# Optimization experiments

Measured on AMD Instinct MI355X. Metric: run time of the kernel, lower is better.

## Reference

```python
import jax, jax.numpy as jnp
import numpy as np

V, E, H, D, A = 10000, 256, 256, 256, 256  # vocab, emb, enc_hid, dec_hid, attn_dim
B, S = 128, 64


def setup_inputs() -> dict:
    key = jax.random.key(0)
    ks = jax.random.split(key, 20)
    rn = lambda k, shp, sc: jax.random.normal(k, shp, jnp.float32) * sc
    tokens = jax.random.randint(ks[0], (B, S), 0, V, dtype=jnp.int32)
    inp = jnp.stack([tokens, jnp.ones_like(tokens)], axis=-1)  # [B,S,2], ch1 = mask
    s = 0.05
    return {
        "input": inp,
        "emb_table": rn(ks[1], (V, E), s),
        "enc_Wih_f": rn(ks[2], (3 * H, E), s), "enc_Whh_f": rn(ks[3], (3 * H, H), s),
        "enc_bih_f": rn(ks[4], (3 * H,), s), "enc_bhh_f": rn(ks[5], (3 * H,), s),
        "enc_Wih_b": rn(ks[6], (3 * H, E), s), "enc_Whh_b": rn(ks[7], (3 * H, H), s),
        "enc_bih_b": rn(ks[8], (3 * H,), s), "enc_bhh_b": rn(ks[9], (3 * H,), s),
        "enc_fc_W": rn(ks[10], (D, 2 * H), s), "enc_fc_b": rn(ks[11], (D,), s),
        "attn_W": rn(ks[12], (A, 2 * H + D), s), "attn_b": rn(ks[13], (A,), s),
        "dec_Wih": rn(ks[14], (3 * D, 2 * H + E), s), "dec_Whh": rn(ks[15], (3 * D, D), s),
        "dec_bih": rn(ks[16], (3 * D,), s), "dec_bhh": rn(ks[17], (3 * D,), s),
        "out_W": rn(ks[18], (V, 2 * H + D + E), s), "out_b": rn(ks[19], (V,), s),
    }


def _gru_cell(xp, h, Whh, bhh):
    # xp = x @ Wih.T + bih already computed; PyTorch gate order r,z,n
    rx, zx, nx = jnp.split(xp, 3, axis=-1)
    rh, zh, nh = jnp.split(h @ Whh.T + bhh, 3, axis=-1)
    r = jax.nn.sigmoid(rx + rh)
    z = jax.nn.sigmoid(zx + zh)
    n = jnp.tanh(nx + r * nh)
    return (1.0 - z) * n + z * h


def _gru_dir(x, Wih, Whh, bih, bhh, reverse):
    # x: [B,S,E] -> outputs [B,S,Hd], final hidden [B,Hd]
    xp = jnp.einsum('bse,ge->bsg', x, Wih) + bih  # [B,S,3Hd]
    Hd = Whh.shape[1]

    def step(h, xpt):
        h = _gru_cell(xpt, h, Whh, bhh)
        return h, h

    h0 = jnp.zeros((x.shape[0], Hd), x.dtype)
    hT, ys = jax.lax.scan(step, h0, jnp.swapaxes(xp, 0, 1), reverse=reverse)
    return jnp.swapaxes(ys, 0, 1), hT


def reference(input, emb_table, enc_Wih_f, enc_Whh_f, enc_bih_f, enc_bhh_f,
              enc_Wih_b, enc_Whh_b, enc_bih_b, enc_bhh_b, enc_fc_W, enc_fc_b,
              attn_W, attn_b, dec_Wih, dec_Whh, dec_bih, dec_bhh, out_W, out_b):
    b, s = input.shape[0], input.shape[1]
    v = emb_table.shape[0]
    tok = input[:, :, 0]
    mask = input[:, :, 1].astype(jnp.float32)
    emb = emb_table[tok] * mask[:, :, None]  # [B,S,E]

    # bidirectional encoder
    f_out, f_h = _gru_dir(emb, enc_Wih_f, enc_Whh_f, enc_bih_f, enc_bhh_f, False)
    b_out, b_h = _gru_dir(emb, enc_Wih_b, enc_Whh_b, enc_bih_b, enc_bhh_b, True)
    enc_out = jnp.concatenate([f_out, b_out], axis=-1)  # [B,S,2H]
    hidden = jnp.tanh(jnp.concatenate([f_h, b_h], axis=-1) @ enc_fc_W.T + enc_fc_b)  # [B,D]

    d = hidden.shape[1]

    def dec_step(carry, _):
        tok_t, h = carry
        e = emb_table[tok_t]  # [B,E]
        rep = jnp.concatenate(
            [jnp.broadcast_to(h[:, None, :], (b, s, d)), enc_out], axis=-1)
        energy = jnp.tanh(jnp.einsum('bsf,af->bsa', rep, attn_W) + attn_b)
        a = jax.nn.softmax(jnp.sum(energy, axis=-1), axis=1)  # [B,S]
        w = jnp.einsum('bs,bsh->bh', a, enc_out)  # [B,2H]
        rnn_in = jnp.concatenate([e, w], axis=-1)
        xp = rnn_in @ dec_Wih.T + dec_bih
        h_new = _gru_cell(xp, h, dec_Whh, dec_bhh)
        logits = jnp.concatenate([h_new, w, e], axis=-1) @ out_W.T + out_b  # [B,V]
        tok_new = jnp.argmax(logits, axis=-1).astype(tok_t.dtype)
        return (tok_new, h_new), logits

    tok0 = jnp.zeros((b,), jnp.int32)
    (_, _), outs = jax.lax.scan(dec_step, (tok0, hidden), None, length=s - 1)
    first = jnp.zeros((b, v), jnp.float32).at[:, 0].set(1.0)  # outputs[:,0] one-hot
    outputs = jnp.concatenate([first[:, None, :], jnp.swapaxes(outs, 0, 1)], axis=1)
    return jax.nn.log_softmax(outputs.reshape(-1, v), axis=-1)
```

## Files before the change

kernel.cpp:

```cpp
#include <hip/hip_runtime.h>
#include <math.h>


__device__ __forceinline__ float dot4(const float4 a, const float4 b) {
    return fmaf(a.x, b.x, fmaf(a.y, b.y, fmaf(a.z, b.z, a.w * b.w)));
}

__global__ void embed_kernel(const int* __restrict__ inp, const float* __restrict__ table,
                             float* __restrict__ emb) {
    int bs = blockIdx.x;
    int tok = inp[bs * 2];
    float msk = (float)inp[bs * 2 + 1];
    emb[bs * 256 + threadIdx.x] = table[tok * 256 + threadIdx.x] * msk;
}

__global__ __launch_bounds__(256) void enc_step_kernel(
    const float* __restrict__ emb,
    const float* __restrict__ Wih_f, const float* __restrict__ Whh_f,
    const float* __restrict__ bih_f, const float* __restrict__ bhh_f,
    const float* __restrict__ Wih_b, const float* __restrict__ Whh_b,
    const float* __restrict__ bih_b, const float* __restrict__ bhh_b,
    const float* __restrict__ hin_f, float* __restrict__ hout_f,
    const float* __restrict__ hin_b, float* __restrict__ hout_b,
    float* __restrict__ enc_out, int step)
{
    const int dir = blockIdx.y;
    const float* Wih = dir ? Wih_b : Wih_f;
    const float* Whh = dir ? Whh_b : Whh_f;
    const float* bih = dir ? bih_b : bih_f;
    const float* bhh = dir ? bhh_b : bhh_f;
    const float* hin = dir ? hin_b : hin_f;
    float* hout = dir ? hout_b : hout_f;
    const int t = dir ? (63 - step) : step;

    const int tid = threadIdx.x;
    const int dl = tid & 31;
    const int bsub = tid >> 5;
    const int d0 = (blockIdx.x & 7) * 32;
    const int b0 = (blockIdx.x >> 3) * 8;
    const int d = d0 + dl;
    const int b = b0 + bsub;

    __shared__ __align__(16) float xs[8][256];
    __shared__ __align__(16) float hs[8][256];
    for (int i = tid; i < 2048; i += 256) {
        int bl = i >> 8, e = i & 255;
        int bb = b0 + bl;
        xs[bl][e] = emb[(bb * 64 + t) * 256 + e];
        hs[bl][e] = hin[bb * 256 + e];
    }
    __syncthreads();

    const float4* x4 = (const float4*)xs[bsub];
    const float4* h4 = (const float4*)hs[bsub];
    const float4* wr_i = (const float4*)(Wih + (size_t)d * 256);
    const float4* wz_i = (const float4*)(Wih + (size_t)(256 + d) * 256);
    const float4* wn_i = (const float4*)(Wih + (size_t)(512 + d) * 256);
    const float4* wr_h = (const float4*)(Whh + (size_t)d * 256);
    const float4* wz_h = (const float4*)(Whh + (size_t)(256 + d) * 256);
    const float4* wn_h = (const float4*)(Whh + (size_t)(512 + d) * 256);

    float rs = 0.f, zs = 0.f, nx = 0.f, nh = 0.f;
    for (int k = 0; k < 64; ++k) {
        float4 xv = x4[k];
        float4 hv = h4[k];
        rs += dot4(xv, wr_i[k]) + dot4(hv, wr_h[k]);
        zs += dot4(xv, wz_i[k]) + dot4(hv, wz_h[k]);
        nx += dot4(xv, wn_i[k]);
        nh += dot4(hv, wn_h[k]);
    }
    rs += bih[d] + bhh[d];
    zs += bih[256 + d] + bhh[256 + d];
    nx += bih[512 + d];
    nh += bhh[512 + d];

    float r = 1.0f / (1.0f + expf(-rs));
    float z = 1.0f / (1.0f + expf(-zs));
    float n = tanhf(nx + r * nh);
    float hprev = hs[bsub][d];
    float hn = (1.0f - z) * n + z * hprev;

    hout[b * 256 + d] = hn;
    enc_out[(b * 64 + t) * 512 + dir * 256 + d] = hn;
}

__global__ __launch_bounds__(256) void enc_fc_kernel(
    const float* __restrict__ hf, const float* __restrict__ hb,
    const float* __restrict__ W, const float* __restrict__ bias,
    float* __restrict__ hdec0)
{
    int b = blockIdx.x, tid = threadIdx.x;
    __shared__ __align__(16) float xs[512];
    xs[tid] = hf[b * 256 + tid];
    xs[256 + tid] = hb[b * 256 + tid];
    __syncthreads();
    const float4* w4 = (const float4*)(W + (size_t)tid * 512);
    const float4* x4 = (const float4*)xs;
    float s = 0.f;
    for (int k = 0; k < 128; ++k) s += dot4(x4[k], w4[k]);
    hdec0[b * 256 + tid] = tanhf(s + bias[tid]);
}

#define GP 68
__global__ __launch_bounds__(256) void gemm2_kernel(
    const float* __restrict__ Amat, int lda,
    const float* __restrict__ Wmat, int ldw,
    const float* __restrict__ bias,
    float* __restrict__ C, long ldc,
    int N, int K)
{
    const int tid = threadIdx.x;
    const int tn = tid & 15;
    const int tm = tid >> 4;
    const long m0 = (long)blockIdx.y * 64;
    const int n0 = blockIdx.x * 64;
    __shared__ __align__(16) float As[64][GP];
    __shared__ __align__(16) float Ws[64][GP];

    const float* Abase = Amat + (m0 + tm) * lda + tn * 4;
    float4 ar[4], wr[4];
    float acc[4][4] = {};

    {
#pragma unroll
        for (int q = 0; q < 4; ++q)
            ar[q] = *(const float4*)(Abase + (long)16 * q * lda);
#pragma unroll
        for (int q = 0; q < 4; ++q) {
            int n = n0 + tm + 16 * q;
            wr[q] = (n < N) ? *(const float4*)(Wmat + (long)n * ldw + tn * 4)
                            : make_float4(0.f, 0.f, 0.f, 0.f);
        }
    }

    int k0 = 0;
    while (true) {
#pragma unroll
        for (int q = 0; q < 4; ++q) {
            *(float4*)&As[tm + 16 * q][tn * 4] = ar[q];
            *(float4*)&Ws[tm + 16 * q][tn * 4] = wr[q];
        }
        __syncthreads();

        const int kn = k0 + 64;
        if (kn < K) {
#pragma unroll
            for (int q = 0; q < 4; ++q)
                ar[q] = *(const float4*)(Abase + (long)16 * q * lda + kn);
#pragma unroll
            for (int q = 0; q < 4; ++q) {
                int n = n0 + tm + 16 * q;
                wr[q] = (n < N) ? *(const float4*)(Wmat + (long)n * ldw + tn * 4 + kn)
                                : make_float4(0.f, 0.f, 0.f, 0.f);
            }
        }

#pragma unroll
        for (int kk = 0; kk < 64; kk += 4) {
            float4 av[4], wv[4];
#pragma unroll
            for (int i = 0; i < 4; ++i) av[i] = *(const float4*)&As[tm + 16 * i][kk];
#pragma unroll
            for (int j = 0; j < 4; ++j) wv[j] = *(const float4*)&Ws[tn + 16 * j][kk];
#pragma unroll
            for (int i = 0; i < 4; ++i)
#pragma unroll
                for (int j = 0; j < 4; ++j)
                    acc[i][j] += dot4(av[i], wv[j]);
        }

        if (kn >= K) break;
        __syncthreads();
        k0 = kn;
    }

#pragma unroll
    for (int i = 0; i < 4; ++i) {
        long m = m0 + tm + 16 * i;
#pragma unroll
        for (int j = 0; j < 4; ++j) {
            int n = n0 + tn + 16 * j;
            if (n < N) C[m * ldc + n] = acc[i][j] + bias[n];
        }
    }
}

__global__ __launch_bounds__(256) void gemm80_kernel(
    const float* __restrict__ Amat, const float* __restrict__ Wmat,
    const float* __restrict__ bias, float* __restrict__ C)
{
    const int tid = threadIdx.x;
    const int tn = tid & 15;
    const int tm = tid >> 4;
    const long m0 = (long)blockIdx.y * 64;
    const int n0 = blockIdx.x * 80;
    __shared__ __align__(16) float As[64][GP];
    __shared__ __align__(16) float Ws[80][GP];

    const float* Abase = Amat + (m0 + tm) * 1024 + tn * 4;
    const float* Wbase = Wmat + (long)(n0 + tm) * 1024 + tn * 4;
    float4 ar[4], wr[5];
    float acc[4][5] = {};

    {
#pragma unroll
        for (int q = 0; q < 4; ++q)
            ar[q] = *(const float4*)(Abase + (long)16 * q * 1024);
#pragma unroll
        for (int q = 0; q < 5; ++q)
            wr[q] = *(const float4*)(Wbase + (long)16 * q * 1024);
    }

    int k0 = 0;
    while (true) {
#pragma unroll
        for (int q = 0; q < 4; ++q)
            *(float4*)&As[tm + 16 * q][tn * 4] = ar[q];
#pragma unroll
        for (int q = 0; q < 5; ++q)
            *(float4*)&Ws[tm + 16 * q][tn * 4] = wr[q];
        __syncthreads();

        const int kn = k0 + 64;
        if (kn < 1024) {
#pragma unroll
            for (int q = 0; q < 4; ++q)
                ar[q] = *(const float4*)(Abase + (long)16 * q * 1024 + kn);
#pragma unroll
            for (int q = 0; q < 5; ++q)
                wr[q] = *(const float4*)(Wbase + (long)16 * q * 1024 + kn);
        }

#pragma unroll
        for (int kk = 0; kk < 64; kk += 4) {
            float4 av[4], wv[5];
#pragma unroll
            for (int i = 0; i < 4; ++i) av[i] = *(const float4*)&As[tm + 16 * i][kk];
#pragma unroll
            for (int j = 0; j < 5; ++j) wv[j] = *(const float4*)&Ws[tn + 16 * j][kk];
#pragma unroll
            for (int i = 0; i < 4; ++i)
#pragma unroll
                for (int j = 0; j < 5; ++j)
                    acc[i][j] += dot4(av[i], wv[j]);
        }

        if (kn >= 1024) break;
        __syncthreads();
        k0 = kn;
    }

#pragma unroll
    for (int i = 0; i < 4; ++i) {
        long m = m0 + tm + 16 * i;
#pragma unroll
        for (int j = 0; j < 5; ++j) {
            int n = n0 + tn + 16 * j;
            C[m * 640000 + n] = acc[i][j] + bias[n];
        }
    }
}

__device__ __forceinline__ void attn_phase(
    int b, const float* __restrict__ hprev, const float* __restrict__ attn_W,
    const float* __restrict__ enc_att, const float* __restrict__ enc_out,
    float* __restrict__ feat,
    float* __restrict__ hsh, float* __restrict__ hE,
    float* __restrict__ part, float* __restrict__ aw)
{
    const int tid = threadIdx.x;
    hsh[tid] = hprev[b * 256 + tid];
    __syncthreads();
    {
        const float4* w4 = (const float4*)(attn_W + (size_t)tid * 768);
        const float4* h4 = (const float4*)hsh;
        float s = 0.f;
        for (int k = 0; k < 64; ++k) s += dot4(h4[k], w4[k]);
        hE[tid] = s;
    }
    __syncthreads();
    {
        const int si = tid & 63, g = tid >> 6;
        const float* ea = enc_att + ((size_t)b * 64 + si) * 256 + g * 64;
        const float* he = hE + g * 64;
        float p = 0.f;
        for (int a = 0; a < 64; ++a) p += tanhf(he[a] + ea[a]);
        part[tid] = p;
    }
    __syncthreads();
    if (tid < 64) {
        float sc = part[tid] + part[64 + tid] + part[128 + tid] + part[192 + tid];
        float m = sc;
        for (int off = 32; off; off >>= 1) m = fmaxf(m, __shfl_xor(m, off));
        float ex = expf(sc - m);
        float sum = ex;
        for (int off = 32; off; off >>= 1) sum += __shfl_xor(sum, off);
        aw[tid] = ex / sum;
    }
    __syncthreads();
    {
        float w0 = 0.f, w1 = 0.f;
        for (int s2 = 0; s2 < 64; ++s2) {
            float as = aw[s2];
            const float* eo = enc_out + ((size_t)b * 64 + s2) * 512;
            w0 = fmaf(as, eo[tid], w0);
            w1 = fmaf(as, eo[256 + tid], w1);
        }
        feat[b * 1024 + 256 + tid] = w0;
        feat[b * 1024 + 512 + tid] = w1;
    }
}

__global__ __launch_bounds__(256) void attn_kernel(
    const float* __restrict__ hprev, const float* __restrict__ attn_W,
    const float* __restrict__ enc_att, const float* __restrict__ enc_out,
    float* __restrict__ feat)
{
    __shared__ __align__(16) float hsh[256];
    __shared__ __align__(16) float hE[256];
    __shared__ __align__(16) float part[256];
    __shared__ __align__(16) float aw[64];
    attn_phase(blockIdx.x, hprev, attn_W, enc_att, enc_out, feat, hsh, hE, part, aw);
}

__device__ __forceinline__ void argmax_phase(
    int b, const float* __restrict__ logits, const float* __restrict__ table,
    int* __restrict__ tok, float* __restrict__ feat,
    float* __restrict__ bv, int* __restrict__ bix)
{
    const int tid = threadIdx.x;
    const float4* row4 = (const float4*)(logits + (long)b * 640000);
    float best = -3.402823466e38f;
    int bi = 0;
    for (int v4 = tid; v4 < 2500; v4 += 256) {
        float4 x = row4[v4];
        int base = v4 << 2;
        if (x.x > best) { best = x.x; bi = base; }
        if (x.y > best) { best = x.y; bi = base + 1; }
        if (x.z > best) { best = x.z; bi = base + 2; }
        if (x.w > best) { best = x.w; bi = base + 3; }
    }
    bv[tid] = best; bix[tid] = bi;
    __syncthreads();
    for (int s2 = 128; s2; s2 >>= 1) {
        if (tid < s2) {
            float o = bv[tid + s2]; int oi = bix[tid + s2];
            if (o > bv[tid] || (o == bv[tid] && oi < bix[tid])) { bv[tid] = o; bix[tid] = oi; }
        }
        __syncthreads();
    }
    int t0 = bix[0];
    if (tid == 0) tok[b] = t0;
    feat[b * 1024 + 768 + tid] = table[(size_t)t0 * 256 + tid];
}

__global__ __launch_bounds__(256) void post_kernel(
    const float* __restrict__ logits, const float* __restrict__ table,
    int* __restrict__ tok, float* __restrict__ feat,
    const float* __restrict__ hcur, const float* __restrict__ attn_W,
    const float* __restrict__ enc_att, const float* __restrict__ enc_out)
{
    __shared__ __align__(16) float s0[256];
    __shared__ __align__(16) float s1[256];
    __shared__ __align__(16) float s2[256];
    __shared__ __align__(16) float s3[64];
    __shared__ __align__(16) int   si[256];
    const int bid = blockIdx.x;
    if (bid < 128)
        argmax_phase(bid, logits, table, tok, feat, s0, si);
    else
        attn_phase(bid - 128, hcur, attn_W, enc_att, enc_out, feat, s0, s1, s2, s3);
}

__global__ __launch_bounds__(256) void dec_gru_kernel(
    const float* __restrict__ feat, const float* __restrict__ hin,
    const float* __restrict__ Wih, const float* __restrict__ Whh,
    const float* __restrict__ bih, const float* __restrict__ bhh,
    float* __restrict__ hout, float* __restrict__ feat_h)
{
    const int tid = threadIdx.x;
    const int dl = tid & 31, bsub = tid >> 5;
    const int d0 = (blockIdx.x & 7) * 32, b0 = (blockIdx.x >> 3) * 8;
    const int d = d0 + dl, b = b0 + bsub;

    __shared__ __align__(16) float rin[8][768];
    __shared__ __align__(16) float hsh[8][256];
    for (int i = tid; i < 2048; i += 256) {
        int bl = i >> 8, k = i & 255;
        rin[bl][k] = feat[(b0 + bl) * 1024 + 768 + k];
    }
    for (int i = tid; i < 4096; i += 256) {
        int bl = i >> 9, k = i & 511;
        rin[bl][256 + k] = feat[(b0 + bl) * 1024 + 256 + k];
    }
    for (int i = tid; i < 2048; i += 256) {
        int bl = i >> 8, k = i & 255;
        hsh[bl][k] = hin[(b0 + bl) * 256 + k];
    }
    __syncthreads();

    const float4* xv4 = (const float4*)rin[bsub];
    const float4* hv4 = (const float4*)hsh[bsub];
    const float4* Wr = (const float4*)(Wih + (size_t)d * 768);
    const float4* Wz = (const float4*)(Wih + (size_t)(256 + d) * 768);
    const float4* Wn = (const float4*)(Wih + (size_t)(512 + d) * 768);
    const float4* Ur = (const float4*)(Whh + (size_t)d * 256);
    const float4* Uz = (const float4*)(Whh + (size_t)(256 + d) * 256);
    const float4* Un = (const float4*)(Whh + (size_t)(512 + d) * 256);

    float rs = 0.f, zs = 0.f, nx = 0.f, nh = 0.f;
    for (int k = 0; k < 192; ++k) {
        float4 xv = xv4[k];
        rs += dot4(xv, Wr[k]);
        zs += dot4(xv, Wz[k]);
        nx += dot4(xv, Wn[k]);
    }
    for (int k = 0; k < 64; ++k) {
        float4 hv = hv4[k];
        rs += dot4(hv, Ur[k]);
        zs += dot4(hv, Uz[k]);
        nh += dot4(hv, Un[k]);
    }
    rs += bih[d] + bhh[d];
    zs += bih[256 + d] + bhh[256 + d];
    nx += bih[512 + d];
    nh += bhh[512 + d];

    float r = 1.0f / (1.0f + expf(-rs));
    float z = 1.0f / (1.0f + expf(-zs));
    float n = tanhf(nx + r * nh);
    float hprev = hsh[bsub][d];
    float hn = (1.0f - z) * n + z * hprev;

    hout[b * 256 + d] = hn;
    feat_h[b * 1024 + d] = hn;
}

__global__ void init_e_kernel(const float* __restrict__ table, float* __restrict__ feat) {
    feat[blockIdx.x * 1024 + 768 + threadIdx.x] = table[threadIdx.x];
}

__global__ __launch_bounds__(256) void logsoftmax_kernel(float* __restrict__ out) {
    const int row = blockIdx.x;
    float* p = out + (long)row * 10000;
    const int tid = threadIdx.x;
    __shared__ float red[256];

    if ((row & 63) == 0) {
        float lse = logf(expf(1.0f) + 9999.0f);
        for (int v = tid; v < 10000; v += 256) p[v] = (v == 0 ? 1.0f : 0.0f) - lse;
        return;
    }

    float vals[40];
    float m = -3.402823466e38f;
#pragma unroll
    for (int i = 0; i < 40; ++i) {
        int v = tid + (i << 8);
        vals[i] = (v < 10000) ? p[v] : -3.402823466e38f;
        m = fmaxf(m, vals[i]);
    }
    red[tid] = m; __syncthreads();
    for (int s2 = 128; s2; s2 >>= 1) { if (tid < s2) red[tid] = fmaxf(red[tid], red[tid + s2]); __syncthreads(); }
    m = red[0]; __syncthreads();

    float sum = 0.f;
#pragma unroll
    for (int i = 0; i < 40; ++i) {
        int v = tid + (i << 8);
        if (v < 10000) sum += expf(vals[i] - m);
    }
    red[tid] = sum; __syncthreads();
    for (int s2 = 128; s2; s2 >>= 1) { if (tid < s2) red[tid] += red[tid + s2]; __syncthreads(); }
    float lse = m + logf(red[0]);

#pragma unroll
    for (int i = 0; i < 40; ++i) {
        int v = tid + (i << 8);
        if (v < 10000) p[v] = vals[i] - lse;
    }
}

extern "C" void kernel_launch(void* const* d_in, const int* in_sizes, int n_in,
                              void* d_out, int out_size, void* d_ws, size_t ws_size,
                              hipStream_t stream)
{
    const int*   inp      = (const int*)d_in[0];
    const float* emb_tab  = (const float*)d_in[1];
    const float* eWih_f   = (const float*)d_in[2];
    const float* eWhh_f   = (const float*)d_in[3];
    const float* ebih_f   = (const float*)d_in[4];
    const float* ebhh_f   = (const float*)d_in[5];
    const float* eWih_b   = (const float*)d_in[6];
    const float* eWhh_b   = (const float*)d_in[7];
    const float* ebih_b   = (const float*)d_in[8];
    const float* ebhh_b   = (const float*)d_in[9];
    const float* fc_W     = (const float*)d_in[10];
    const float* fc_b     = (const float*)d_in[11];
    const float* attn_W   = (const float*)d_in[12];
    const float* attn_b   = (const float*)d_in[13];
    const float* dWih     = (const float*)d_in[14];
    const float* dWhh     = (const float*)d_in[15];
    const float* dbih     = (const float*)d_in[16];
    const float* dbhh     = (const float*)d_in[17];
    const float* out_W    = (const float*)d_in[18];
    const float* out_b    = (const float*)d_in[19];

    float* ws = (float*)d_ws;
    float* emb     = ws;
    float* enc_out = emb + 2097152;
    float* enc_att = enc_out + 4194304;
    float* hf      = enc_att + 2097152;
    float* hb      = hf + 65536;
    float* hdec    = hb + 65536;
    float* feat    = hdec + 65536;
    int*   tok     = (int*)(feat + 131072);
    float* out     = (float*)d_out;

    embed_kernel<<<8192, 256, 0, stream>>>(inp, emb_tab, emb);
    hipMemsetAsync(hf, 0, 32768 * sizeof(float), stream);
    hipMemsetAsync(hb, 0, 32768 * sizeof(float), stream);
    for (int i = 0; i < 64; ++i) {
        const float* hinf = hf + (i & 1) * 32768;
        float* houtf = hf + ((i + 1) & 1) * 32768;
        const float* hinb = hb + (i & 1) * 32768;
        float* houtb = hb + ((i + 1) & 1) * 32768;
        enc_step_kernel<<<dim3(128, 2), 256, 0, stream>>>(
            emb, eWih_f, eWhh_f, ebih_f, ebhh_f, eWih_b, eWhh_b, ebih_b, ebhh_b,
            hinf, houtf, hinb, houtb, enc_out, i);
    }
    enc_fc_kernel<<<128, 256, 0, stream>>>(hf, hb, fc_W, fc_b, hdec);

    gemm2_kernel<<<dim3(4, 128), 256, 0, stream>>>(
        enc_out, 512, attn_W + 256, 768, attn_b, enc_att, 256, 256, 512);

    init_e_kernel<<<128, 256, 0, stream>>>(emb_tab, feat);
    attn_kernel<<<128, 256, 0, stream>>>(hdec, attn_W, enc_att, enc_out, feat);

    for (int t = 1; t < 64; ++t) {
        const float* hprev = hdec + ((t - 1) & 1) * 32768;
        float* hcur = hdec + (t & 1) * 32768;
        dec_gru_kernel<<<128, 256, 0, stream>>>(feat, hprev, dWih, dWhh, dbih, dbhh, hcur, feat);
        gemm80_kernel<<<dim3(125, 2), 256, 0, stream>>>(
            feat, out_W, out_b, out + (long)t * 10000);
        if (t < 63)
            post_kernel<<<256, 256, 0, stream>>>(
                out + (long)t * 10000, emb_tab, tok, feat,
                hcur, attn_W, enc_att, enc_out);
    }

    logsoftmax_kernel<<<8192, 256, 0, stream>>>(out);
}
```

Baseline: 17.46 ms.

## Persist encoder loop in one kernel and fuse argmax/attention into output GEMM

The 64 per-step encoder launches plus the embed kernel are replaced by one persistent kernel per direction and batch pair, which keeps the hidden state in shared memory and gathers embeddings inline. In the decoder, the separate post kernel is removed: argmax is folded into the output GEMM epilogue as packed 64-bit keys combined with atomicMax, and the attention phase runs as extra blocks in the same launch, writing to a double-buffered feature array. The next GRU step decodes the token from these slots and resets them, cutting launches per step from three to two. The cost is an encoder with only 128 blocks that each loop serially over all steps while rereading weights from global memory.

```diff
diff --git a/kernel.cpp b/kernel.cpp
--- a/kernel.cpp
+++ b/kernel.cpp
@@ -6,53 +6,33 @@
     return fmaf(a.x, b.x, fmaf(a.y, b.y, fmaf(a.z, b.z, a.w * b.w)));
 }
 
-__global__ void embed_kernel(const int* __restrict__ inp, const float* __restrict__ table,
-                             float* __restrict__ emb) {
-    int bs = blockIdx.x;
-    int tok = inp[bs * 2];
-    float msk = (float)inp[bs * 2 + 1];
-    emb[bs * 256 + threadIdx.x] = table[tok * 256 + threadIdx.x] * msk;
-}
-
-__global__ __launch_bounds__(256) void enc_step_kernel(
-    const float* __restrict__ emb,
+__global__ __launch_bounds__(512) void enc_loop_kernel(
+    const int* __restrict__ inp, const float* __restrict__ table,
     const float* __restrict__ Wih_f, const float* __restrict__ Whh_f,
     const float* __restrict__ bih_f, const float* __restrict__ bhh_f,
     const float* __restrict__ Wih_b, const float* __restrict__ Whh_b,
     const float* __restrict__ bih_b, const float* __restrict__ bhh_b,
-    const float* __restrict__ hin_f, float* __restrict__ hout_f,
-    const float* __restrict__ hin_b, float* __restrict__ hout_b,
-    float* __restrict__ enc_out, int step)
-{
-    const int dir = blockIdx.y;
+    float* __restrict__ hf, float* __restrict__ hb,
+    float* __restrict__ enc_out)
+{
+    const int bid = blockIdx.x;
+    const int dir = bid >> 6;
+    const int b0  = (bid & 63) * 2;
     const float* Wih = dir ? Wih_b : Wih_f;
     const float* Whh = dir ? Whh_b : Whh_f;
     const float* bih = dir ? bih_b : bih_f;
     const float* bhh = dir ? bhh_b : bhh_f;
-    const float* hin = dir ? hin_b : hin_f;
-    float* hout = dir ? hout_b : hout_f;
-    const int t = dir ? (63 - step) : step;
-
-    const int tid = threadIdx.x;
-    const int dl = tid & 31;
-    const int bsub = tid >> 5;
-    const int d0 = (blockIdx.x & 7) * 32;
-    const int b0 = (blockIdx.x >> 3) * 8;
-    const int d = d0 + dl;
-    const int b = b0 + bsub;
-
-    __shared__ __align__(16) float xs[8][256];
-    __shared__ __align__(16) float hs[8][256];
-    for (int i = tid; i < 2048; i += 256) {
-        int bl = i >> 8, e = i & 255;
-        int bb = b0 + bl;
-        xs[bl][e] = emb[(bb * 64 + t) * 256 + e];
-        hs[bl][e] = hin[bb * 256 + e];
-    }
-    __syncthreads();
-
-    const float4* x4 = (const float4*)xs[bsub];
-    const float4* h4 = (const float4*)hs[bsub];
+
+    const int tid  = threadIdx.x;
+    const int d    = tid & 255;
+    const int bsel = tid >> 8;
+    const int b    = b0 + bsel;
+
+    __shared__ __align__(16) float xs[2][256];
+    __shared__ __align__(16) float hs[2][2][256];
+
+    hs[0][bsel][d] = 0.f;
+
     const float4* wr_i = (const float4*)(Wih + (size_t)d * 256);
     const float4* wz_i = (const float4*)(Wih + (size_t)(256 + d) * 256);
     const float4* wn_i = (const float4*)(Wih + (size_t)(512 + d) * 256);
@@ -60,28 +40,50 @@
     const float4* wz_h = (const float4*)(Whh + (size_t)(256 + d) * 256);
     const float4* wn_h = (const float4*)(Whh + (size_t)(512 + d) * 256);
 
-    float rs = 0.f, zs = 0.f, nx = 0.f, nh = 0.f;
-    for (int k = 0; k < 64; ++k) {
-        float4 xv = x4[k];
-        float4 hv = h4[k];
-        rs += dot4(xv, wr_i[k]) + dot4(hv, wr_h[k]);
-        zs += dot4(xv, wz_i[k]) + dot4(hv, wz_h[k]);
-        nx += dot4(xv, wn_i[k]);
-        nh += dot4(hv, wn_h[k]);
-    }
-    rs += bih[d] + bhh[d];
-    zs += bih[256 + d] + bhh[256 + d];
-    nx += bih[512 + d];
-    nh += bhh[512 + d];
-
-    float r = 1.0f / (1.0f + expf(-rs));
-    float z = 1.0f / (1.0f + expf(-zs));
-    float n = tanhf(nx + r * nh);
-    float hprev = hs[bsub][d];
-    float hn = (1.0f - z) * n + z * hprev;
-
-    hout[b * 256 + d] = hn;
-    enc_out[(b * 64 + t) * 512 + dir * 256 + d] = hn;
+    const float br = bih[d] + bhh[d];
+    const float bz = bih[256 + d] + bhh[256 + d];
+    const float bnx = bih[512 + d];
+    const float bnh = bhh[512 + d];
+
+    float hn = 0.f;
+    int cur = 0;
+    for (int step = 0; step < 64; ++step) {
+        const int t = dir ? (63 - step) : step;
+        __syncthreads();
+        {
+            int tok = inp[(b * 64 + t) * 2];
+            float msk = (float)inp[(b * 64 + t) * 2 + 1];
+            xs[bsel][d] = table[(size_t)tok * 256 + d] * msk;
+        }
+        __syncthreads();
+
+        const float4* x4 = (const float4*)xs[bsel];
+        const float4* h4 = (const float4*)hs[cur][bsel];
+        float rs = 0.f, zs = 0.f, nx = 0.f, nh = 0.f;
+        for (int k = 0; k < 64; ++k) {
+            float4 xv = x4[k];
+            float4 hv = h4[k];
+            rs += dot4(xv, wr_i[k]) + dot4(hv, wr_h[k]);
+            zs += dot4(xv, wz_i[k]) + dot4(hv, wz_h[k]);
+            nx += dot4(xv, wn_i[k]);
+            nh += dot4(hv, wn_h[k]);
+        }
+        rs += br;
+        zs += bz;
+        nx += bnx;
+        nh += bnh;
+
+        float r = 1.0f / (1.0f + expf(-rs));
+        float z = 1.0f / (1.0f + expf(-zs));
+        float n = tanhf(nx + r * nh);
+        float hprev = hs[cur][bsel][d];
+        hn = (1.0f - z) * n + z * hprev;
+
+        hs[cur ^ 1][bsel][d] = hn;
+        enc_out[(b * 64 + t) * 512 + dir * 256 + d] = hn;
+        cur ^= 1;
+    }
+    (dir ? hb : hf)[b * 256 + d] = hn;
 }
 
 __global__ __launch_bounds__(256) void enc_fc_kernel(
@@ -185,86 +187,10 @@
     }
 }
 
-__global__ __launch_bounds__(256) void gemm80_kernel(
-    const float* __restrict__ Amat, const float* __restrict__ Wmat,
-    const float* __restrict__ bias, float* __restrict__ C)
-{
-    const int tid = threadIdx.x;
-    const int tn = tid & 15;
-    const int tm = tid >> 4;
-    const long m0 = (long)blockIdx.y * 64;
-    const int n0 = blockIdx.x * 80;
-    __shared__ __align__(16) float As[64][GP];
-    __shared__ __align__(16) float Ws[80][GP];
-
-    const float* Abase = Amat + (m0 + tm) * 1024 + tn * 4;
-    const float* Wbase = Wmat + (long)(n0 + tm) * 1024 + tn * 4;
-    float4 ar[4], wr[5];
-    float acc[4][5] = {};
-
-    {
-#pragma unroll
-        for (int q = 0; q < 4; ++q)
-            ar[q] = *(const float4*)(Abase + (long)16 * q * 1024);
-#pragma unroll
-        for (int q = 0; q < 5; ++q)
-            wr[q] = *(const float4*)(Wbase + (long)16 * q * 1024);
-    }
-
-    int k0 = 0;
-    while (true) {
-#pragma unroll
-        for (int q = 0; q < 4; ++q)
-            *(float4*)&As[tm + 16 * q][tn * 4] = ar[q];
-#pragma unroll
-        for (int q = 0; q < 5; ++q)
-            *(float4*)&Ws[tm + 16 * q][tn * 4] = wr[q];
-        __syncthreads();
-
-        const int kn = k0 + 64;
-        if (kn < 1024) {
-#pragma unroll
-            for (int q = 0; q < 4; ++q)
-                ar[q] = *(const float4*)(Abase + (long)16 * q * 1024 + kn);
-#pragma unroll
-            for (int q = 0; q < 5; ++q)
-                wr[q] = *(const float4*)(Wbase + (long)16 * q * 1024 + kn);
-        }
-
-#pragma unroll
-        for (int kk = 0; kk < 64; kk += 4) {
-            float4 av[4], wv[5];
-#pragma unroll
-            for (int i = 0; i < 4; ++i) av[i] = *(const float4*)&As[tm + 16 * i][kk];
-#pragma unroll
-            for (int j = 0; j < 5; ++j) wv[j] = *(const float4*)&Ws[tn + 16 * j][kk];
-#pragma unroll
-            for (int i = 0; i < 4; ++i)
-#pragma unroll
-                for (int j = 0; j < 5; ++j)
-                    acc[i][j] += dot4(av[i], wv[j]);
-        }
-
-        if (kn >= 1024) break;
-        __syncthreads();
-        k0 = kn;
-    }
-
-#pragma unroll
-    for (int i = 0; i < 4; ++i) {
-        long m = m0 + tm + 16 * i;
-#pragma unroll
-        for (int j = 0; j < 5; ++j) {
-            int n = n0 + tn + 16 * j;
-            C[m * 640000 + n] = acc[i][j] + bias[n];
-        }
-    }
-}
-
 __device__ __forceinline__ void attn_phase(
     int b, const float* __restrict__ hprev, const float* __restrict__ attn_W,
     const float* __restrict__ enc_att, const float* __restrict__ enc_out,
-    float* __restrict__ feat,
+    float* __restrict__ feat_tgt,
     float* __restrict__ hsh, float* __restrict__ hE,
     float* __restrict__ part, float* __restrict__ aw)
 {
@@ -306,92 +232,57 @@
             w0 = fmaf(as, eo[tid], w0);
             w1 = fmaf(as, eo[256 + tid], w1);
         }
-        feat[b * 1024 + 256 + tid] = w0;
-        feat[b * 1024 + 512 + tid] = w1;
+        feat_tgt[b * 1024 + 256 + tid] = w0;
+        feat_tgt[b * 1024 + 512 + tid] = w1;
     }
 }
 
 __global__ __launch_bounds__(256) void attn_kernel(
     const float* __restrict__ hprev, const float* __restrict__ attn_W,
     const float* __restrict__ enc_att, const float* __restrict__ enc_out,
-    float* __restrict__ feat)
+    float* __restrict__ feat_tgt)
 {
     __shared__ __align__(16) float hsh[256];
     __shared__ __align__(16) float hE[256];
     __shared__ __align__(16) float part[256];
     __shared__ __align__(16) float aw[64];
-    attn_phase(blockIdx.x, hprev, attn_W, enc_att, enc_out, feat, hsh, hE, part, aw);
-}
-
-__device__ __forceinline__ void argmax_phase(
-    int b, const float* __restrict__ logits, const float* __restrict__ table,
-    int* __restrict__ tok, float* __restrict__ feat,
-    float* __restrict__ bv, int* __restrict__ bix)
-{
-    const int tid = threadIdx.x;
-    const float4* row4 = (const float4*)(logits + (long)b * 640000);
-    float best = -3.402823466e38f;
-    int bi = 0;
-    for (int v4 = tid; v4 < 2500; v4 += 256) {
-        float4 x = row4[v4];
-        int base = v4 << 2;
-        if (x.x > best) { best = x.x; bi = base; }
-        if (x.y > best) { best = x.y; bi = base + 1; }
-        if (x.z > best) { best = x.z; bi = base + 2; }
-        if (x.w > best) { best = x.w; bi = base + 3; }
-    }
-    bv[tid] = best; bix[tid] = bi;
-    __syncthreads();
-    for (int s2 = 128; s2; s2 >>= 1) {
-        if (tid < s2) {
-            float o = bv[tid + s2]; int oi = bix[tid + s2];
-            if (o > bv[tid] || (o == bv[tid] && oi < bix[tid])) { bv[tid] = o; bix[tid] = oi; }
-        }
-        __syncthreads();
-    }
-    int t0 = bix[0];
-    if (tid == 0) tok[b] = t0;
-    feat[b * 1024 + 768 + tid] = table[(size_t)t0 * 256 + tid];
-}
-
-__global__ __launch_bounds__(256) void post_kernel(
-    const float* __restrict__ logits, const float* __restrict__ table,
-    int* __restrict__ tok, float* __restrict__ feat,
-    const float* __restrict__ hcur, const float* __restrict__ attn_W,
-    const float* __restrict__ enc_att, const float* __restrict__ enc_out)
-{
-    __shared__ __align__(16) float s0[256];
-    __shared__ __align__(16) float s1[256];
-    __shared__ __align__(16) float s2[256];
-    __shared__ __align__(16) float s3[64];
-    __shared__ __align__(16) int   si[256];
-    const int bid = blockIdx.x;
-    if (bid < 128)
-        argmax_phase(bid, logits, table, tok, feat, s0, si);
-    else
-        attn_phase(bid - 128, hcur, attn_W, enc_att, enc_out, feat, s0, s1, s2, s3);
+    attn_phase(blockIdx.x, hprev, attn_W, enc_att, enc_out, feat_tgt, hsh, hE, part, aw);
 }
 
 __global__ __launch_bounds__(256) void dec_gru_kernel(
-    const float* __restrict__ feat, const float* __restrict__ hin,
+    const float* __restrict__ emb_tab, float* __restrict__ fb,
+    const float* __restrict__ hin,
+    const unsigned long long* __restrict__ slots_read,
+    unsigned long long* __restrict__ slots_reset,
     const float* __restrict__ Wih, const float* __restrict__ Whh,
     const float* __restrict__ bih, const float* __restrict__ bhh,
-    float* __restrict__ hout, float* __restrict__ feat_h)
+    float* __restrict__ hout)
 {
     const int tid = threadIdx.x;
     const int dl = tid & 31, bsub = tid >> 5;
     const int d0 = (blockIdx.x & 7) * 32, b0 = (blockIdx.x >> 3) * 8;
     const int d = d0 + dl, b = b0 + bsub;
 
+    if (tid == 0) slots_reset[blockIdx.x] = 0ull;
+
     __shared__ __align__(16) float rin[8][768];
     __shared__ __align__(16) float hsh[8][256];
+
+    const bool ewrite = ((blockIdx.x & 7) == 0);
     for (int i = tid; i < 2048; i += 256) {
         int bl = i >> 8, k = i & 255;
-        rin[bl][k] = feat[(b0 + bl) * 1024 + 768 + k];
+        int tk = 0;
+        if (slots_read) {
+            unsigned long long s = slots_read[b0 + bl];
+            tk = (int)(~((unsigned int)(s & 0xFFFFFFFFull)));
+        }
+        float v = emb_tab[(size_t)tk * 256 + k];
+        rin[bl][k] = v;
+        if (ewrite) fb[(b0 + bl) * 1024 + 768 + k] = v;
     }
     for (int i = tid; i < 4096; i += 256) {
         int bl = i >> 9, k = i & 511;
-        rin[bl][256 + k] = feat[(b0 + bl) * 1024 + 256 + k];
+        rin[bl][256 + k] = fb[(b0 + bl) * 1024 + 256 + k];
     }
     for (int i = tid; i < 2048; i += 256) {
         int bl = i >> 8, k = i & 255;
@@ -433,11 +324,117 @@
     float hn = (1.0f - z) * n + z * hprev;
 
     hout[b * 256 + d] = hn;
-    feat_h[b * 1024 + d] = hn;
-}
-
-__global__ void init_e_kernel(const float* __restrict__ table, float* __restrict__ feat) {
-    feat[blockIdx.x * 1024 + 768 + threadIdx.x] = table[threadIdx.x];
+    fb[b * 1024 + d] = hn;
+}
+
+__global__ __launch_bounds__(256) void mega_kernel(
+    const float* __restrict__ fb, const float* __restrict__ Wmat,
+    const float* __restrict__ bias, float* __restrict__ C,
+    unsigned long long* __restrict__ slots_write,
+    float* __restrict__ fnext,
+    const float* __restrict__ hcur, const float* __restrict__ attn_W,
+    const float* __restrict__ enc_att, const float* __restrict__ enc_out)
+{
+    __shared__ __align__(16) float As[64][GP];
+    __shared__ __align__(16) float Ws[80][GP];
+    __shared__ __align__(16) unsigned long long keys[64][16];
+    __shared__ __align__(16) float a0[256];
+    __shared__ __align__(16) float a1[256];
+    __shared__ __align__(16) float a2[256];
+    __shared__ __align__(16) float a3[64];
+
+    const int bid = blockIdx.x;
+    if (bid >= 250) {
+        attn_phase(bid - 250, hcur, attn_W, enc_att, enc_out, fnext, a0, a1, a2, a3);
+        return;
+    }
+
+    const int tid = threadIdx.x;
+    const int tn = tid & 15;
+    const int tm = tid >> 4;
+    const long m0 = (long)(bid & 1) * 64;
+    const int n0 = (bid >> 1) * 80;
+
+    const float* Abase = fb + (m0 + tm) * 1024 + tn * 4;
+    const float* Wbase = Wmat + (long)(n0 + tm) * 1024 + tn * 4;
+    float4 ar[4], wr[5];
+    float acc[4][5] = {};
+
+    {
+#pragma unroll
+        for (int q = 0; q < 4; ++q)
+            ar[q] = *(const float4*)(Abase + (long)16 * q * 1024);
+#pragma unroll
+        for (int q = 0; q < 5; ++q)
+            wr[q] = *(const float4*)(Wbase + (long)16 * q * 1024);
+    }
+
+    int k0 = 0;
+    while (true) {
+#pragma unroll
+        for (int q = 0; q < 4; ++q)
+            *(float4*)&As[tm + 16 * q][tn * 4] = ar[q];
+#pragma unroll
+        for (int q = 0; q < 5; ++q)
+            *(float4*)&Ws[tm + 16 * q][tn * 4] = wr[q];
+        __syncthreads();
+
+        const int kn = k0 + 64;
+        if (kn < 1024) {
+#pragma unroll
+            for (int q = 0; q < 4; ++q)
+                ar[q] = *(const float4*)(Abase + (long)16 * q * 1024 + kn);
+#pragma unroll
+            for (int q = 0; q < 5; ++q)
+                wr[q] = *(const float4*)(Wbase + (long)16 * q * 1024 + kn);
+        }
+
+#pragma unroll
+        for (int kk = 0; kk < 64; kk += 4) {
+            float4 av[4], wv[5];
+#pragma unroll
+            for (int i = 0; i < 4; ++i) av[i] = *(const float4*)&As[tm + 16 * i][kk];
+#pragma unroll
+            for (int j = 0; j < 5; ++j) wv[j] = *(const float4*)&Ws[tn + 16 * j][kk];
+#pragma unroll
+            for (int i = 0; i < 4; ++i)
+#pragma unroll
+                for (int j = 0; j < 5; ++j)
+                    acc[i][j] += dot4(av[i], wv[j]);
+        }
+
+        if (kn >= 1024) break;
+        __syncthreads();
+        k0 = kn;
+    }
+
+#pragma unroll
+    for (int i = 0; i < 4; ++i) {
+        long m = m0 + tm + 16 * i;
+        unsigned long long best = 0ull;
+#pragma unroll
+        for (int j = 0; j < 5; ++j) {
+            int n = n0 + tn + 16 * j;
+            float v = acc[i][j] + bias[n];
+            C[m * 640000 + n] = v;
+            unsigned int bits = __float_as_uint(v);
+            unsigned int ov = (bits & 0x80000000u) ? ~bits : (bits | 0x80000000u);
+            unsigned long long key =
+                ((unsigned long long)ov << 32) | (unsigned int)(~(unsigned int)n);
+            if (key > best) best = key;
+        }
+        keys[tm + 16 * i][tn] = best;
+    }
+    __syncthreads();
+    if (tid < 64) {
+        unsigned long long best = keys[tid][0];
+#pragma unroll
+        for (int q = 1; q < 16; ++q) {
+            unsigned long long k2 = keys[tid][q];
+            if (k2 > best) best = k2;
+        }
+        atomicMax(&slots_write[m0 + tid], best);
+    }
 }
 
 __global__ __launch_bounds__(256) void logsoftmax_kernel(float* __restrict__ out) {
@@ -507,46 +504,40 @@
     const float* out_b    = (const float*)d_in[19];
 
     float* ws = (float*)d_ws;
-    float* emb     = ws;
-    float* enc_out = emb + 2097152;
+    float* enc_out = ws;
     float* enc_att = enc_out + 4194304;
     float* hf      = enc_att + 2097152;
-    float* hb      = hf + 65536;
-    float* hdec    = hb + 65536;
+    float* hb      = hf + 32768;
+    float* hdec    = hb + 32768;
     float* feat    = hdec + 65536;
-    int*   tok     = (int*)(feat + 131072);
+    unsigned long long* slots = (unsigned long long*)(feat + 262144);
     float* out     = (float*)d_out;
 
-    embed_kernel<<<8192, 256, 0, stream>>>(inp, emb_tab, emb);
-    hipMemsetAsync(hf, 0, 32768 * sizeof(float), stream);
-    hipMemsetAsync(hb, 0, 32768 * sizeof(float), stream);
-    for (int i = 0; i < 64; ++i) {
-        const float* hinf = hf + (i & 1) * 32768;
-        float* houtf = hf + ((i + 1) & 1) * 32768;
-        const float* hinb = hb + (i & 1) * 32768;
-        float* houtb = hb + ((i + 1) & 1) * 32768;
-        enc_step_kernel<<<dim3(128, 2), 256, 0, stream>>>(
-            emb, eWih_f, eWhh_f, ebih_f, ebhh_f, eWih_b, eWhh_b, ebih_b, ebhh_b,
-            hinf, houtf, hinb, houtb, enc_out, i);
-    }
+    enc_loop_kernel<<<128, 512, 0, stream>>>(
+        inp, emb_tab, eWih_f, eWhh_f, ebih_f, ebhh_f,
+        eWih_b, eWhh_b, ebih_b, ebhh_b, hf, hb, enc_out);
     enc_fc_kernel<<<128, 256, 0, stream>>>(hf, hb, fc_W, fc_b, hdec);
 
     gemm2_kernel<<<dim3(4, 128), 256, 0, stream>>>(
         enc_out, 512, attn_W + 256, 768, attn_b, enc_att, 256, 256, 512);
 
-    init_e_kernel<<<128, 256, 0, stream>>>(emb_tab, feat);
-    attn_kernel<<<128, 256, 0, stream>>>(hdec, attn_W, enc_att, enc_out, feat);
+    attn_kernel<<<128, 256, 0, stream>>>(hdec, attn_W, enc_att, enc_out, feat + 131072);
 
     for (int t = 1; t < 64; ++t) {
+        float* fb    = feat + (t & 1) * 131072;
+        float* fnext = feat + ((t + 1) & 1) * 131072;
         const float* hprev = hdec + ((t - 1) & 1) * 32768;
         float* hcur = hdec + (t & 1) * 32768;
-        dec_gru_kernel<<<128, 256, 0, stream>>>(feat, hprev, dWih, dWhh, dbih, dbhh, hcur, feat);
-        gemm80_kernel<<<dim3(125, 2), 256, 0, stream>>>(
-            feat, out_W, out_b, out + (long)t * 10000);
-        if (t < 63)
-            post_kernel<<<256, 256, 0, stream>>>(
-                out + (long)t * 10000, emb_tab, tok, feat,
-                hcur, attn_W, enc_att, enc_out);
+        const unsigned long long* slots_read =
+            (t == 1) ? nullptr : slots + ((t - 1) & 1) * 128;
+        unsigned long long* slots_cur = slots + (t & 1) * 128;
+
+        dec_gru_kernel<<<128, 256, 0, stream>>>(
+            emb_tab, fb, hprev, slots_read, slots_cur,
+            dWih, dWhh, dbih, dbhh, hcur);
+        mega_kernel<<<378, 256, 0, stream>>>(
+            fb, out_W, out_b, out + (long)t * 10000, slots_cur,
+            fnext, hcur, attn_W, enc_att, enc_out);
     }
 
     logsoftmax_kernel<<<8192, 256, 0, stream>>>(out);
```

Result: slower. 20.43 ms (+17.1%).
